# Optimization experiments

Measured on AMD Instinct MI355X. Metric: run time of the kernel, lower is better.

The kernel has to match this reference:

```python
import jax, jax.numpy as jnp
import numpy as np

N_NODES = 100000
N_EDGES = 1600000
IN_CH = 6
EDGE_FEAT = 8


def glorot(key, shape):
    lim = np.sqrt(6.0 / (shape[0] + shape[1]))
    return jax.random.uniform(key, shape, jnp.float32, -lim, lim)


def setup_inputs() -> dict:
    key = jax.random.key(0)
    ks = jax.random.split(key, 10)
    x = jax.random.normal(ks[0], (N_NODES, IN_CH), jnp.float32)
    edge_index = jax.random.randint(ks[1], (2, N_EDGES), 0, N_NODES, jnp.int64)
    edge_attr = jax.random.normal(ks[2], (N_EDGES, EDGE_FEAT), jnp.float32)
    return {
        "x": x,
        "edge_index": edge_index,
        "edge_attr": edge_attr,
        "W1": glorot(ks[3], (IN_CH, 32)), "b1": jnp.zeros((32,), jnp.float32),
        "W2": glorot(ks[4], (32, 16)), "b2": jnp.zeros((16,), jnp.float32),
        "W3": glorot(ks[5], (16 * 2 + EDGE_FEAT, 32)), "b3": jnp.zeros((32,), jnp.float32),
        "W4": glorot(ks[6], (32, 1)), "b4": jnp.zeros((1,), jnp.float32),
    }


def gcn_conv(x, src, dst, W, b, n_nodes):
    # PyG GCNConv: add self-loops, symmetric deg^{-1/2} normalization,
    # linear transform, scatter-add aggregation over incoming edges, bias.
    h = x @ W  # [N, out]
    deg = jnp.zeros((n_nodes,), h.dtype).at[dst].add(1.0) + 1.0  # +1 self-loop
    dinv = jax.lax.rsqrt(deg)  # [N]
    norm = dinv[src] * dinv[dst]  # [E]
    msg = h[src] * norm[:, None]  # gather + scale
    agg = jnp.zeros_like(h).at[dst].add(msg)
    agg = agg + h * (dinv * dinv)[:, None]  # self-loop term
    return agg + b


def reference(x, edge_index, edge_attr, W1, b1, W2, b2, W3, b3, W4, b4):
    src, dst = edge_index[0], edge_index[1]
    n = x.shape[0]
    h = jax.nn.relu(gcn_conv(x, src, dst, W1, b1, n))
    h = jax.nn.relu(gcn_conv(h, src, dst, W2, b2, n))
    # edge gather-concat-MLP
    edge_input = jnp.concatenate([h[src], h[dst], edge_attr], axis=1)  # [E, 40]
    out = jax.nn.relu(edge_input @ W3 + b3) @ W4 + b4  # [E, 1]
    return out.squeeze(-1)
```

## Files before the change

### kernel.cpp

```cpp
#include <hip/hip_runtime.h>


constexpr int TPB = 256;
constexpr int NB = 256;
constexpr int BSH = 8;
constexpr int MAXB = 1024;
constexpr int EDGE_ITERS = 8;

using short8  = __attribute__((ext_vector_type(8))) short;
using f32x16  = __attribute__((ext_vector_type(16))) float;
using uintx4  = __attribute__((ext_vector_type(4))) unsigned;
using floatx4 = __attribute__((ext_vector_type(4))) float;

__device__ __forceinline__ void nt_store4(uint4 v, uint4* p) {
    uintx4 e = {v.x, v.y, v.z, v.w};
    __builtin_nontemporal_store(e, reinterpret_cast<uintx4*>(p));
}
__device__ __forceinline__ float4 nt_load_f4(const float4* p) {
    floatx4 e = __builtin_nontemporal_load(reinterpret_cast<const floatx4*>(p));
    return float4{e.x, e.y, e.z, e.w};
}

__device__ __forceinline__ float bf_lo(unsigned w) {
    return __builtin_bit_cast(float, (unsigned)(w << 16));
}
__device__ __forceinline__ float bf_hi(unsigned w) {
    return __builtin_bit_cast(float, w & 0xFFFF0000u);
}
__device__ __forceinline__ unsigned bf1(float f) {
    unsigned u = __builtin_bit_cast(unsigned, f);
    return (u + 0x7FFFu + ((u >> 16) & 1u)) >> 16;
}
__device__ __forceinline__ unsigned pk(float lo, float hi) {
    return bf1(lo) | (bf1(hi) << 16);
}
__device__ __forceinline__ void unp8(uint4 v, float* o) {
    o[0] = bf_lo(v.x); o[1] = bf_hi(v.x); o[2] = bf_lo(v.y); o[3] = bf_hi(v.y);
    o[4] = bf_lo(v.z); o[5] = bf_hi(v.z); o[6] = bf_lo(v.w); o[7] = bf_hi(v.w);
}
__device__ __forceinline__ void unp6(uint4 v, float* o) {
    o[0] = bf_lo(v.x); o[1] = bf_hi(v.x); o[2] = bf_lo(v.y); o[3] = bf_hi(v.y);
    o[4] = bf_lo(v.z); o[5] = bf_hi(v.z);
}

__global__ void k_bhist(const int* __restrict__ dst, unsigned* __restrict__ histG,
                        int E, int B, int CH) {
    __shared__ unsigned h[MAXB];
    for (int t = threadIdx.x; t < B; t += blockDim.x) h[t] = 0;
    __syncthreads();
    int b = blockIdx.x;
    int beg = b * CH, end = min(E, beg + CH);
    for (int i = beg + threadIdx.x; i < end; i += blockDim.x)
        atomicAdd(&h[__builtin_nontemporal_load(dst + i) >> BSH], 1u);
    __syncthreads();
    for (int t = threadIdx.x; t < B; t += blockDim.x) histG[b * B + t] = h[t];
}

__global__ void k_scan1t(const unsigned* __restrict__ histG, unsigned* __restrict__ bsum,
                         int M, int B) {
    __shared__ unsigned s[TPB];
    int tid = threadIdx.x;
    int i = blockIdx.x * TPB + tid;
    unsigned v = (i < M) ? histG[(i % NB) * B + (i / NB)] : 0u;
    s[tid] = v;
    __syncthreads();
    for (int ofs = TPB / 2; ofs > 0; ofs >>= 1) {
        if (tid < ofs) s[tid] += s[tid + ofs];
        __syncthreads();
    }
    if (tid == 0) bsum[blockIdx.x] = s[0];
}

__global__ void k_scan2(unsigned* __restrict__ bsum, int nb) {
    __shared__ unsigned s[512];
    int tid = threadIdx.x;
    unsigned v = (tid < nb) ? bsum[tid] : 0u;
    s[tid] = v;
    __syncthreads();
    for (int ofs = 1; ofs < 512; ofs <<= 1) {
        unsigned t = (tid >= ofs) ? s[tid - ofs] : 0u;
        __syncthreads();
        s[tid] += t;
        __syncthreads();
    }
    if (tid < nb) bsum[tid] = s[tid] - v;
}

__global__ void k_scan3t(const unsigned* __restrict__ histG, const unsigned* __restrict__ bsum,
                         unsigned* __restrict__ scannedM, int M, int B) {
    __shared__ unsigned s[TPB];
    int tid = threadIdx.x;
    int i = blockIdx.x * TPB + tid;
    unsigned v = (i < M) ? histG[(i % NB) * B + (i / NB)] : 0u;
    s[tid] = v;
    __syncthreads();
    for (int ofs = 1; ofs < TPB; ofs <<= 1) {
        unsigned t = (tid >= ofs) ? s[tid - ofs] : 0u;
        __syncthreads();
        s[tid] += t;
        __syncthreads();
    }
    if (i < M) scannedM[i] = bsum[blockIdx.x] + s[tid] - v;
}

__global__ void k_bscatter(const int* __restrict__ src, const int* __restrict__ dst,
                           const unsigned* __restrict__ scannedM, unsigned* __restrict__ lvl1,
                           int E, int B, int CH) {
    __shared__ unsigned cur[MAXB];
    int b = blockIdx.x;
    for (int t = threadIdx.x; t < B; t += blockDim.x) cur[t] = scannedM[t * NB + b];
    __syncthreads();
    int beg = b * CH, end = min(E, beg + CH);
    for (int i = beg + threadIdx.x; i < end; i += blockDim.x) {
        int d = __builtin_nontemporal_load(dst + i);
        int sv = __builtin_nontemporal_load(src + i);
        int bk = d >> BSH;
        unsigned p = atomicAdd(&cur[bk], 1u);
        lvl1[p] = ((unsigned)sv << BSH) | (unsigned)(d & ((1 << BSH) - 1));
    }
}

__global__ void k_bbuild(const unsigned* __restrict__ lvl1, const unsigned* __restrict__ scannedM,
                         const float* __restrict__ x, unsigned* __restrict__ rowptr,
                         float* __restrict__ dinv, uint4* __restrict__ xs,
                         int* __restrict__ csr_src, int N, int E, int B) {
    __shared__ unsigned cnt[1 << BSH];
    __shared__ unsigned ro[1 << BSH];
    int b = blockIdx.x;
    int tid = threadIdx.x;
    unsigned gbase = scannedM[(size_t)b * NB];
    unsigned gend = (b + 1 < B) ? scannedM[(size_t)(b + 1) * NB] : (unsigned)E;
    cnt[tid] = 0;
    __syncthreads();
    for (unsigned i = gbase + tid; i < gend; i += (unsigned)blockDim.x)
        atomicAdd(&cnt[lvl1[i] & ((1u << BSH) - 1u)], 1u);
    __syncthreads();
    unsigned v = cnt[tid];
    ro[tid] = v;
    __syncthreads();
    for (int ofs = 1; ofs < (1 << BSH); ofs <<= 1) {
        unsigned t = (tid >= ofs) ? ro[tid - ofs] : 0u;
        __syncthreads();
        ro[tid] += t;
        __syncthreads();
    }
    unsigned excl = ro[tid] - v;
    int n = (b << BSH) + tid;
    if (n < N) {
        rowptr[n] = gbase + excl;
        float di = rsqrtf((float)v + 1.0f);
        dinv[n] = di;
        const float* xr = x + (size_t)n * 6;
        uint4 o;
        o.x = pk(xr[0] * di, xr[1] * di);
        o.y = pk(xr[2] * di, xr[3] * di);
        o.z = pk(xr[4] * di, xr[5] * di);
        o.w = 0u;
        xs[n] = o;
        if (n == N - 1) rowptr[N] = gend;
    }
    __syncthreads();
    cnt[tid] = gbase + excl;
    __syncthreads();
    for (unsigned i = gbase + tid; i < gend; i += (unsigned)blockDim.x) {
        unsigned w = lvl1[i];
        unsigned p = atomicAdd(&cnt[w & ((1u << BSH) - 1u)], 1u);
        csr_src[p] = (int)(w >> BSH);
    }
}

__global__ void k_gagg6f(const unsigned* __restrict__ rowptr, const int* __restrict__ csr_src,
                         const float* __restrict__ dinv, const uint4* __restrict__ xs,
                         const float* __restrict__ W1, const float* __restrict__ b1,
                         const float* __restrict__ W2, uint4* __restrict__ hs2, int N) {
    int gid = blockIdx.x * blockDim.x + threadIdx.x;
    int n = gid >> 3, q = gid & 7;
    if (n >= N) return;
    unsigned beg = rowptr[n], end = rowptr[n + 1];
    float acc[6] = {0.f, 0.f, 0.f, 0.f, 0.f, 0.f};
    unsigned j0 = beg + q;
    if (j0 < end) {
        auto cidx = [&](unsigned jj) {
            return __builtin_nontemporal_load(csr_src + (jj < end ? jj : end - 1));
        };
        int i1 = cidx(j0 + 8);
        uint4 g0 = xs[cidx(j0)];
        for (unsigned j = j0; j < end; j += 8) {
            int i2 = cidx(j + 16);
            uint4 g1 = xs[i1];
            float t[6];
            unp6(g0, t);
#pragma unroll
            for (int i = 0; i < 6; ++i) acc[i] += t[i];
            g0 = g1; i1 = i2;
        }
    }
#pragma unroll
    for (int i = 0; i < 6; ++i) {
        acc[i] += __shfl_xor(acc[i], 1);
        acc[i] += __shfl_xor(acc[i], 2);
        acc[i] += __shfl_xor(acc[i], 4);
    }
    float t6[6];
    unp6(xs[n], t6);
#pragma unroll
    for (int i = 0; i < 6; ++i) acc[i] += t6[i];
    float di = dinv[n];
    float h1[4];
#pragma unroll
    for (int cc = 0; cc < 4; ++cc) {
        int oc = q * 4 + cc;
        float s = 0.f;
#pragma unroll
        for (int k = 0; k < 6; ++k) s = fmaf(acc[k], W1[k * 32 + oc], s);
        h1[cc] = fmaxf(fmaf(s, di, b1[oc]), 0.f);
    }
    float z[16];
#pragma unroll
    for (int j = 0; j < 16; ++j) z[j] = 0.f;
#pragma unroll
    for (int cc = 0; cc < 4; ++cc) {
        int c = q * 4 + cc;
        float a = h1[cc];
#pragma unroll
        for (int j = 0; j < 16; ++j) z[j] = fmaf(a, W2[c * 16 + j], z[j]);
    }
#pragma unroll
    for (int j = 0; j < 16; ++j) {
        z[j] += __shfl_xor(z[j], 1);
        z[j] += __shfl_xor(z[j], 2);
        z[j] += __shfl_xor(z[j], 4);
    }
    if (q < 2) {
        unsigned w[4];
#pragma unroll
        for (int p = 0; p < 4; ++p)
            w[p] = pk(z[q * 8 + 2 * p] * di, z[q * 8 + 2 * p + 1] * di);
        nt_store4(uint4{w[0], w[1], w[2], w[3]}, hs2 + (size_t)n * 2 + q);
    }
}

__global__ void k_gagg16(const unsigned* __restrict__ rowptr, const int* __restrict__ csr_src,
                         const float* __restrict__ dinv, const uint4* __restrict__ hs2,
                         const float* __restrict__ b2, uint4* __restrict__ h2, int N) {
    int gid = blockIdx.x * blockDim.x + threadIdx.x;
    int n = gid >> 4, q = gid & 15;
    int h = q & 1, e8 = q >> 1;
    if (n >= N) return;
    unsigned beg = rowptr[n], end = rowptr[n + 1];
    float acc[8] = {0.f, 0.f, 0.f, 0.f, 0.f, 0.f, 0.f, 0.f};
    unsigned j0 = beg + e8;
    if (j0 < end) {
        auto cidx = [&](unsigned jj) {
            return __builtin_nontemporal_load(csr_src + (jj < end ? jj : end - 1));
        };
        int i1 = cidx(j0 + 8);
        uint4 g0 = hs2[(size_t)cidx(j0) * 2 + h];
        for (unsigned j = j0; j < end; j += 8) {
            int i2 = cidx(j + 16);
            uint4 g1 = hs2[(size_t)i1 * 2 + h];
            float t[8];
            unp8(g0, t);
#pragma unroll
            for (int i = 0; i < 8; ++i) acc[i] += t[i];
            g0 = g1; i1 = i2;
        }
    }
#pragma unroll
    for (int i = 0; i < 8; ++i) {
        acc[i] += __shfl_xor(acc[i], 2);
        acc[i] += __shfl_xor(acc[i], 4);
        acc[i] += __shfl_xor(acc[i], 8);
    }
    if (e8) return;
    float t8[8];
    unp8(hs2[(size_t)n * 2 + h], t8);
    float di = dinv[n];
    unsigned w[4];
#pragma unroll
    for (int i = 0; i < 4; ++i) {
        float r0 = fmaxf(fmaf(acc[2 * i] + t8[2 * i], di, b2[h * 8 + 2 * i]), 0.f);
        float r1 = fmaxf(fmaf(acc[2 * i + 1] + t8[2 * i + 1], di, b2[h * 8 + 2 * i + 1]), 0.f);
        w[i] = pk(r0, r1);
    }
    h2[(size_t)n * 2 + h] = uint4{w[0], w[1], w[2], w[3]};
}

__global__ void k_wprep(const float* __restrict__ W3, const float* __restrict__ b3,
                        uint4* __restrict__ w3tab) {
    int lane = threadIdx.x;
    if (lane >= 64) return;
    int j = lane & 31, hi = lane >> 5;
#pragma unroll
    for (int s = 0; s < 3; ++s) {
        unsigned w[4];
#pragma unroll
        for (int p = 0; p < 4; ++p) {
            int k0 = s * 16 + hi * 8 + 2 * p;
            float f0 = (k0 < 40) ? W3[k0 * 32 + j] : (k0 == 40 ? b3[j] : 0.f);
            float f1 = (k0 + 1 < 40) ? W3[(k0 + 1) * 32 + j] : 0.f;
            w[p] = pk(f0, f1);
        }
        w3tab[lane * 3 + s] = uint4{w[0], w[1], w[2], w[3]};
    }
}

__global__ void __launch_bounds__(TPB) k_edge_mfma(
    const int* __restrict__ src, const int* __restrict__ dst,
    const uint4* __restrict__ h2, const float* __restrict__ eattr,
    const uint4* __restrict__ w3tab, const float* __restrict__ W4,
    const float* __restrict__ b4, float* __restrict__ out, int E) {
    const int lane = threadIdx.x & 63;
    const int wave = threadIdx.x >> 6;
    const int e31 = lane & 31;
    const int hi = lane >> 5;

    short8 wA0, wA1, wA2;
    {
        const uint4* wt = w3tab + (size_t)lane * 3;
        wA0 = __builtin_bit_cast(short8, wt[0]);
        wA1 = __builtin_bit_cast(short8, wt[1]);
        wA2 = __builtin_bit_cast(short8, wt[2]);
    }
    const float4* W4v = reinterpret_cast<const float4*>(W4);
    const float4 w4q0 = W4v[hi], w4q1 = W4v[2 + hi], w4q2 = W4v[4 + hi], w4q3 = W4v[6 + hi];
    const float b4v = b4[0];
    const long base0 = ((long)blockIdx.x * 4 + wave) * (32L * EDGE_ITERS);

    const uint4 one_u = (hi == 1) ? uint4{0x3F80u, 0u, 0u, 0u} : uint4{0u, 0u, 0u, 0u};
    const short8 one_s8 = __builtin_bit_cast(short8, one_u);

    auto eclamp = [&](int it) -> size_t {
        long et = base0 + (long)it * 32 + e31;
        return (size_t)(et < E ? et : (long)(E - 1));
    };
    auto load_a2 = [&](int it) -> short8 {
        if (hi != 0) return one_s8;
        const float4* ea = reinterpret_cast<const float4*>(eattr + eclamp(it) * 8);
        float4 e0 = nt_load_f4(ea);
        float4 e1 = nt_load_f4(ea + 1);
        return __builtin_bit_cast(short8, uint4{pk(e0.x, e0.y), pk(e0.z, e0.w),
                                                pk(e1.x, e1.y), pk(e1.z, e1.w)});
    };

    int is[EDGE_ITERS], id[EDGE_ITERS];
#pragma unroll
    for (int it = 0; it < EDGE_ITERS; ++it) {
        is[it] = __builtin_nontemporal_load(src + eclamp(it));
        id[it] = __builtin_nontemporal_load(dst + eclamp(it));
    }

    uint4 hsA = h2[(size_t)is[0] * 2 + hi], hdA = h2[(size_t)id[0] * 2 + hi];
    short8 a2A = load_a2(0);
    uint4 hsB = h2[(size_t)is[1] * 2 + hi], hdB = h2[(size_t)id[1] * 2 + hi];
    short8 a2B = load_a2(1);

#pragma unroll
    for (int it = 0; it < EDGE_ITERS; ++it) {
        uint4 hsC{0u, 0u, 0u, 0u}, hdC{0u, 0u, 0u, 0u};
        short8 a2C = one_s8;
        if (it + 2 < EDGE_ITERS) {
            hsC = h2[(size_t)is[it + 2] * 2 + hi];
            hdC = h2[(size_t)id[it + 2] * 2 + hi];
            a2C = load_a2(it + 2);
        }

        f32x16 c;
#pragma unroll
        for (int i = 0; i < 16; ++i) c[i] = 0.f;
        c = __builtin_amdgcn_mfma_f32_32x32x16_bf16(wA0, __builtin_bit_cast(short8, hsA), c, 0, 0, 0);
        c = __builtin_amdgcn_mfma_f32_32x32x16_bf16(wA1, __builtin_bit_cast(short8, hdA), c, 0, 0, 0);
        c = __builtin_amdgcn_mfma_f32_32x32x16_bf16(wA2, a2A, c, 0, 0, 0);

        float z = 0.f;
#pragma unroll
        for (int r = 0; r < 4; ++r) {
            z = fmaf(fmaxf(c[0 * 4 + r], 0.f), ((const float*)&w4q0)[r], z);
            z = fmaf(fmaxf(c[1 * 4 + r], 0.f), ((const float*)&w4q1)[r], z);
            z = fmaf(fmaxf(c[2 * 4 + r], 0.f), ((const float*)&w4q2)[r], z);
            z = fmaf(fmaxf(c[3 * 4 + r], 0.f), ((const float*)&w4q3)[r], z);
        }
        z += __shfl_xor(z, 32);
        long erow = base0 + (long)it * 32 + e31;
        if (hi == 0 && erow < E) __builtin_nontemporal_store(z + b4v, out + erow);

        hsA = hsB; hdA = hdB; a2A = a2B;
        hsB = hsC; hdB = hdC; a2B = a2C;
    }
}

extern "C" void kernel_launch(void* const* d_in, const int* in_sizes, int n_in,
                              void* d_out, int out_size, void* d_ws, size_t ws_size,
                              hipStream_t stream) {
    const float* x     = (const float*)d_in[0];
    const int*   ei    = (const int*)d_in[1];
    const float* eattr = (const float*)d_in[2];
    const float* W1 = (const float*)d_in[3];
    const float* b1 = (const float*)d_in[4];
    const float* W2 = (const float*)d_in[5];
    const float* b2 = (const float*)d_in[6];
    const float* W3 = (const float*)d_in[7];
    const float* b3 = (const float*)d_in[8];
    const float* W4 = (const float*)d_in[9];
    const float* b4 = (const float*)d_in[10];
    float* out = (float*)d_out;

    const int N = in_sizes[0] / 6;
    const int E = in_sizes[2] / 8;
    const int* src = ei;
    const int* dst = ei + E;

    const int B  = (N + (1 << BSH) - 1) >> BSH;
    const int CH = (E + NB - 1) / NB;
    const int M  = B * NB;
    const int nbM = (M + TPB - 1) / TPB;

    char* wsb = (char*)d_ws;
    size_t off = 0;
    auto alloc4 = [&](size_t elems) {
        void* p = wsb + off;
        off += ((elems * 4 + 15) & ~(size_t)15);
        return p;
    };
    unsigned* rowptr   = (unsigned*)alloc4(N + 1);
    float*    dinv     = (float*)alloc4(N);
    unsigned* bsum     = (unsigned*)alloc4(512);
    unsigned* histG    = (unsigned*)alloc4((size_t)NB * B);
    unsigned* scannedM = (unsigned*)alloc4((size_t)NB * B);
    int*      csr_src  = (int*)alloc4(E);
    unsigned* big      = (unsigned*)alloc4((size_t)N * 16 > (size_t)E ? (size_t)N * 16 : (size_t)E);
    uint4*    xs       = (uint4*)alloc4((size_t)N * 4);
    uint4*    w3tab    = (uint4*)alloc4(64 * 3 * 4);

    unsigned* lvl1 = big;
    uint4*    hs2  = (uint4*)big;
    uint4*    h2   = (uint4*)(big + (size_t)N * 8);

    k_wprep<<<1, 64, 0, stream>>>(W3, b3, w3tab);

    k_bhist   <<<NB, TPB, 0, stream>>>(dst, histG, E, B, CH);
    k_scan1t  <<<nbM, TPB, 0, stream>>>(histG, bsum, M, B);
    k_scan2   <<<1, 512, 0, stream>>>(bsum, nbM);
    k_scan3t  <<<nbM, TPB, 0, stream>>>(histG, bsum, scannedM, M, B);
    k_bscatter<<<NB, TPB, 0, stream>>>(src, dst, scannedM, lvl1, E, B, CH);
    k_bbuild  <<<B, 1 << BSH, 0, stream>>>(lvl1, scannedM, x, rowptr, dinv, xs, csr_src, N, E, B);

    k_gagg6f<<<((size_t)N * 8 + TPB - 1) / TPB, TPB, 0, stream>>>(
        rowptr, csr_src, dinv, xs, W1, b1, W2, hs2, N);

    k_gagg16<<<((size_t)N * 16 + TPB - 1) / TPB, TPB, 0, stream>>>(
        rowptr, csr_src, dinv, hs2, b2, h2, N);

    const long per_block = 4L * 32 * EDGE_ITERS;
    const int eblocks = (int)((E + per_block - 1) / per_block);
    k_edge_mfma<<<eblocks, TPB, 0, stream>>>(src, dst, (const uint4*)h2, eattr,
                                             (const uint4*)w3tab, W4, b4, out, E);
}
```

Before: 169.1 us.

## Cut edges per wave, split MFMA accumulators, redundantly compute layer-1 per lane

The edge MLP kernel now handles 2 tiles of 32 edges per wave instead of 8, giving many more blocks and dropping the deep software prefetch. The MFMA chain is split into two independent accumulators to shorten the dependency chain. In the first aggregation kernel each of the 8 lanes now computes all 32 layer-1 outputs and directly produces 2 of the 16 layer-2 outputs. This removes the 48 cross-lane shuffles and lets all lanes store 4-byte results, at the cost of redundant FMAs and more registers. The csr index loads there also switch from nontemporal to plain loads.

```diff
diff --git a/kernel.cpp b/kernel.cpp
--- a/kernel.cpp
+++ b/kernel.cpp
@@ -5,7 +5,6 @@
 constexpr int NB = 256;
 constexpr int BSH = 8;
 constexpr int MAXB = 1024;
-constexpr int EDGE_ITERS = 8;
 
 using short8  = __attribute__((ext_vector_type(8))) short;
 using f32x16  = __attribute__((ext_vector_type(16))) float;
@@ -172,7 +171,7 @@
 __global__ void k_gagg6f(const unsigned* __restrict__ rowptr, const int* __restrict__ csr_src,
                          const float* __restrict__ dinv, const uint4* __restrict__ xs,
                          const float* __restrict__ W1, const float* __restrict__ b1,
-                         const float* __restrict__ W2, uint4* __restrict__ hs2, int N) {
+                         const float* __restrict__ W2, unsigned* __restrict__ hs2w, int N) {
     int gid = blockIdx.x * blockDim.x + threadIdx.x;
     int n = gid >> 3, q = gid & 7;
     if (n >= N) return;
@@ -181,7 +180,7 @@
     unsigned j0 = beg + q;
     if (j0 < end) {
         auto cidx = [&](unsigned jj) {
-            return __builtin_nontemporal_load(csr_src + (jj < end ? jj : end - 1));
+            return csr_src[jj < end ? jj : end - 1];
         };
         int i1 = cidx(j0 + 8);
         uint4 g0 = xs[cidx(j0)];
@@ -206,38 +205,22 @@
 #pragma unroll
     for (int i = 0; i < 6; ++i) acc[i] += t6[i];
     float di = dinv[n];
-    float h1[4];
-#pragma unroll
-    for (int cc = 0; cc < 4; ++cc) {
-        int oc = q * 4 + cc;
+    float h1[32];
+#pragma unroll
+    for (int oc = 0; oc < 32; ++oc) {
         float s = 0.f;
 #pragma unroll
         for (int k = 0; k < 6; ++k) s = fmaf(acc[k], W1[k * 32 + oc], s);
-        h1[cc] = fmaxf(fmaf(s, di, b1[oc]), 0.f);
-    }
-    float z[16];
-#pragma unroll
-    for (int j = 0; j < 16; ++j) z[j] = 0.f;
-#pragma unroll
-    for (int cc = 0; cc < 4; ++cc) {
-        int c = q * 4 + cc;
-        float a = h1[cc];
-#pragma unroll
-        for (int j = 0; j < 16; ++j) z[j] = fmaf(a, W2[c * 16 + j], z[j]);
-    }
-#pragma unroll
-    for (int j = 0; j < 16; ++j) {
-        z[j] += __shfl_xor(z[j], 1);
-        z[j] += __shfl_xor(z[j], 2);
-        z[j] += __shfl_xor(z[j], 4);
-    }
-    if (q < 2) {
-        unsigned w[4];
-#pragma unroll
-        for (int p = 0; p < 4; ++p)
-            w[p] = pk(z[q * 8 + 2 * p] * di, z[q * 8 + 2 * p + 1] * di);
-        nt_store4(uint4{w[0], w[1], w[2], w[3]}, hs2 + (size_t)n * 2 + q);
-    }
+        h1[oc] = fmaxf(fmaf(s, di, b1[oc]), 0.f);
+    }
+    int j0c = 2 * q;
+    float z0 = 0.f, z1 = 0.f;
+#pragma unroll
+    for (int c = 0; c < 32; ++c) {
+        z0 = fmaf(h1[c], W2[c * 16 + j0c], z0);
+        z1 = fmaf(h1[c], W2[c * 16 + j0c + 1], z1);
+    }
+    __builtin_nontemporal_store(pk(z0 * di, z1 * di), hs2w + (size_t)n * 8 + q);
 }
 
 __global__ void k_gagg16(const unsigned* __restrict__ rowptr, const int* __restrict__ csr_src,
@@ -325,7 +308,7 @@
     const float4* W4v = reinterpret_cast<const float4*>(W4);
     const float4 w4q0 = W4v[hi], w4q1 = W4v[2 + hi], w4q2 = W4v[4 + hi], w4q3 = W4v[6 + hi];
     const float b4v = b4[0];
-    const long base0 = ((long)blockIdx.x * 4 + wave) * (32L * EDGE_ITERS);
+    const long base0 = ((long)blockIdx.x * 4 + wave) * 64L;
 
     const uint4 one_u = (hi == 1) ? uint4{0x3F80u, 0u, 0u, 0u} : uint4{0u, 0u, 0u, 0u};
     const short8 one_s8 = __builtin_bit_cast(short8, one_u);
@@ -343,50 +326,36 @@
                                                 pk(e1.x, e1.y), pk(e1.z, e1.w)});
     };
 
-    int is[EDGE_ITERS], id[EDGE_ITERS];
-#pragma unroll
-    for (int it = 0; it < EDGE_ITERS; ++it) {
-        is[it] = __builtin_nontemporal_load(src + eclamp(it));
-        id[it] = __builtin_nontemporal_load(dst + eclamp(it));
-    }
-
-    uint4 hsA = h2[(size_t)is[0] * 2 + hi], hdA = h2[(size_t)id[0] * 2 + hi];
-    short8 a2A = load_a2(0);
-    uint4 hsB = h2[(size_t)is[1] * 2 + hi], hdB = h2[(size_t)id[1] * 2 + hi];
-    short8 a2B = load_a2(1);
-
-#pragma unroll
-    for (int it = 0; it < EDGE_ITERS; ++it) {
-        uint4 hsC{0u, 0u, 0u, 0u}, hdC{0u, 0u, 0u, 0u};
-        short8 a2C = one_s8;
-        if (it + 2 < EDGE_ITERS) {
-            hsC = h2[(size_t)is[it + 2] * 2 + hi];
-            hdC = h2[(size_t)id[it + 2] * 2 + hi];
-            a2C = load_a2(it + 2);
-        }
-
-        f32x16 c;
-#pragma unroll
-        for (int i = 0; i < 16; ++i) c[i] = 0.f;
-        c = __builtin_amdgcn_mfma_f32_32x32x16_bf16(wA0, __builtin_bit_cast(short8, hsA), c, 0, 0, 0);
-        c = __builtin_amdgcn_mfma_f32_32x32x16_bf16(wA1, __builtin_bit_cast(short8, hdA), c, 0, 0, 0);
-        c = __builtin_amdgcn_mfma_f32_32x32x16_bf16(wA2, a2A, c, 0, 0, 0);
-
+    int is0 = __builtin_nontemporal_load(src + eclamp(0));
+    int id0 = __builtin_nontemporal_load(dst + eclamp(0));
+    int is1 = __builtin_nontemporal_load(src + eclamp(1));
+    int id1 = __builtin_nontemporal_load(dst + eclamp(1));
+    uint4 hs0 = h2[(size_t)is0 * 2 + hi], hd0 = h2[(size_t)id0 * 2 + hi];
+    uint4 hs1 = h2[(size_t)is1 * 2 + hi], hd1 = h2[(size_t)id1 * 2 + hi];
+    short8 a20 = load_a2(0);
+    short8 a21 = load_a2(1);
+
+    auto tile = [&](uint4 hs, uint4 hd, short8 a2, int it) {
+        f32x16 cA, cB;
+#pragma unroll
+        for (int i = 0; i < 16; ++i) { cA[i] = 0.f; cB[i] = 0.f; }
+        cA = __builtin_amdgcn_mfma_f32_32x32x16_bf16(wA0, __builtin_bit_cast(short8, hs), cA, 0, 0, 0);
+        cB = __builtin_amdgcn_mfma_f32_32x32x16_bf16(wA2, a2, cB, 0, 0, 0);
+        cA = __builtin_amdgcn_mfma_f32_32x32x16_bf16(wA1, __builtin_bit_cast(short8, hd), cA, 0, 0, 0);
         float z = 0.f;
 #pragma unroll
         for (int r = 0; r < 4; ++r) {
-            z = fmaf(fmaxf(c[0 * 4 + r], 0.f), ((const float*)&w4q0)[r], z);
-            z = fmaf(fmaxf(c[1 * 4 + r], 0.f), ((const float*)&w4q1)[r], z);
-            z = fmaf(fmaxf(c[2 * 4 + r], 0.f), ((const float*)&w4q2)[r], z);
-            z = fmaf(fmaxf(c[3 * 4 + r], 0.f), ((const float*)&w4q3)[r], z);
+            z = fmaf(fmaxf(cA[0 * 4 + r] + cB[0 * 4 + r], 0.f), ((const float*)&w4q0)[r], z);
+            z = fmaf(fmaxf(cA[1 * 4 + r] + cB[1 * 4 + r], 0.f), ((const float*)&w4q1)[r], z);
+            z = fmaf(fmaxf(cA[2 * 4 + r] + cB[2 * 4 + r], 0.f), ((const float*)&w4q2)[r], z);
+            z = fmaf(fmaxf(cA[3 * 4 + r] + cB[3 * 4 + r], 0.f), ((const float*)&w4q3)[r], z);
         }
         z += __shfl_xor(z, 32);
         long erow = base0 + (long)it * 32 + e31;
         if (hi == 0 && erow < E) __builtin_nontemporal_store(z + b4v, out + erow);
-
-        hsA = hsB; hdA = hdB; a2A = a2B;
-        hsB = hsC; hdB = hdC; a2B = a2C;
-    }
+    };
+    tile(hs0, hd0, a20, 0);
+    tile(hs1, hd1, a21, 1);
 }
 
 extern "C" void kernel_launch(void* const* d_in, const int* in_sizes, int n_in,
@@ -446,13 +415,12 @@
     k_bbuild  <<<B, 1 << BSH, 0, stream>>>(lvl1, scannedM, x, rowptr, dinv, xs, csr_src, N, E, B);
 
     k_gagg6f<<<((size_t)N * 8 + TPB - 1) / TPB, TPB, 0, stream>>>(
-        rowptr, csr_src, dinv, xs, W1, b1, W2, hs2, N);
+        rowptr, csr_src, dinv, xs, W1, b1, W2, (unsigned*)hs2, N);
 
     k_gagg16<<<((size_t)N * 16 + TPB - 1) / TPB, TPB, 0, stream>>>(
         rowptr, csr_src, dinv, hs2, b2, h2, N);
 
-    const long per_block = 4L * 32 * EDGE_ITERS;
-    const int eblocks = (int)((E + per_block - 1) / per_block);
+    const int eblocks = (E + 255) / 256;
     k_edge_mfma<<<eblocks, TPB, 0, stream>>>(src, dst, (const uint4*)h2, eattr,
                                              (const uint4*)w3tab, W4, b4, out, E);
 }
```

Measured after the change: 149.8 us. 1.13x faster.
